# Performance work log

Hardware: AMD Instinct MI355X
Metric: run time of the kernel (lower is better)

Reference implementation:

```python
import jax, jax.numpy as jnp
import numpy as np

N_NODES = 100000
N_EDGES = 1200000
N_GRAPHS = 2048
VOCAB = 10000
D = 64
C = 2


def setup_inputs() -> dict:
    key = jax.random.key(0)
    ks = jax.random.split(key, 12)
    x = jax.random.randint(ks[0], (N_NODES,), 0, VOCAB)
    edge_index = jax.random.randint(ks[1], (2, N_EDGES), 0, N_NODES)
    batch = jnp.sort(jax.random.randint(ks[2], (N_NODES,), 0, N_GRAPHS))
    s = 0.1
    return {
        'x': x,
        'edge_index': edge_index,
        'batch': batch,
        'emb': jax.random.normal(ks[3], (VOCAB, D), jnp.float32) * s,
        'W1l': jax.random.normal(ks[4], (D, D), jnp.float32) * s,
        'b1l': jnp.zeros((D,), jnp.float32),
        'W1r': jax.random.normal(ks[5], (D, D), jnp.float32) * s,
        'W2l': jax.random.normal(ks[6], (D, D), jnp.float32) * s,
        'b2l': jnp.zeros((D,), jnp.float32),
        'W2r': jax.random.normal(ks[7], (D, D), jnp.float32) * s,
        'Wout': jax.random.normal(ks[8], (C, D), jnp.float32) * s,
        'bout': jnp.zeros((C,), jnp.float32),
    }


def _sage(h, src, dst, Wl, bl, Wr, n_nodes):
    # mean aggregation of source messages onto target nodes (PyG SAGEConv, aggr='mean')
    agg = jax.ops.segment_sum(h[src], dst, num_segments=n_nodes)  # [N, D]
    cnt = jax.ops.segment_sum(jnp.ones((src.shape[0],), h.dtype), dst, num_segments=n_nodes)
    agg = agg / jnp.maximum(cnt, 1.0)[:, None]
    # lin_l(agg) + lin_r(root); lin_l carries the bias, lin_r has none
    return agg @ Wl.T + bl + h @ Wr.T


def reference(x, edge_index, batch, emb, W1l, b1l, W1r, W2l, b2l, W2r, Wout, bout):
    src, dst = edge_index[0], edge_index[1]
    h = emb[x]                                   # [N, D] embedding lookup
    h = jax.nn.relu(_sage(h, src, dst, W1l, b1l, W1r, N_NODES))
    h = jax.nn.relu(_sage(h, src, dst, W2l, b2l, W2r, N_NODES))
    # global mean pool per graph
    pooled = jax.ops.segment_sum(h, batch, num_segments=N_GRAPHS)
    gcnt = jax.ops.segment_sum(jnp.ones((N_NODES,), h.dtype), batch, num_segments=N_GRAPHS)
    pooled = pooled / jnp.maximum(gcnt, 1.0)[:, None]
    return pooled @ Wout.T + bout                # [G, C]
```

## Files before the change

### kernel.cpp

```cpp
#include <hip/hip_runtime.h>

#define NN 100000
#define NE 1200000
#define NG 2048
#define VOCAB 10000
#define D 64
#define C 2

#define NBK 196
#define BSH 9
#define SLOT 7168

typedef _Float16 half8 __attribute__((ext_vector_type(8)));
typedef _Float16 half2 __attribute__((ext_vector_type(2)));

#if __has_builtin(__builtin_amdgcn_fdot2)
#define FDOT2(a, b, c) __builtin_amdgcn_fdot2((a), (b), (c), false)
#else
#define FDOT2(a, b, c) ((float)(a)[0] * (float)(b)[0] + (float)(a)[1] * (float)(b)[1] + (c))
#endif

__device__ __forceinline__ int atomAddI(int* p, int v) {
    return __hip_atomic_fetch_add(p, v, __ATOMIC_RELAXED, __HIP_MEMORY_SCOPE_AGENT);
}
__device__ __forceinline__ void atomAddF(float* p, float v) {
    __hip_atomic_fetch_add(p, v, __ATOMIC_RELAXED, __HIP_MEMORY_SCOPE_AGENT);
}

__global__ void __launch_bounds__(256) k_prep(const float4* __restrict__ emb4,
        half8* __restrict__ embh,
        const float* __restrict__ W1l, const float* __restrict__ W1r,
        const float* __restrict__ W2l, const float* __restrict__ W2r,
        half2* __restrict__ wp,
        const int* __restrict__ batch, int* __restrict__ gs) {
    int blk = blockIdx.x;
    if (blk < 313) {
        int i = blk * 256 + threadIdx.x;
        if (i >= VOCAB * 8) return;
        float4 a = emb4[(size_t)i * 2], b = emb4[(size_t)i * 2 + 1];
        half8 h;
        h[0] = (_Float16)a.x; h[1] = (_Float16)a.y; h[2] = (_Float16)a.z; h[3] = (_Float16)a.w;
        h[4] = (_Float16)b.x; h[5] = (_Float16)b.y; h[6] = (_Float16)b.z; h[7] = (_Float16)b.w;
        embh[i] = h;
    } else if (blk < 345) {
        int i = (blk - 313) * 256 + threadIdx.x;
        if (i >= 4 * 2048) return;
        int mat = i >> 11, idx = i & 2047;
        const float* W = (mat == 0) ? W1l : (mat == 1) ? W1r : (mat == 2) ? W2l : W2r;
        int row = idx >> 5, kk = idx & 31;
        half2 o;
        o[0] = (_Float16)W[row * 64 + 2 * kk];
        o[1] = (_Float16)W[row * 64 + 2 * kk + 1];
        wp[i] = o;
    } else {
        int n = (blk - 345) * 256 + threadIdx.x;
        if (n >= NN) return;
        int b = batch[n];
        if (n == 0) {
            for (int g = 0; g <= b; ++g) gs[g] = 0;
        } else {
            int bp = batch[n - 1];
            for (int g = bp + 1; g <= b; ++g) gs[g] = n;
        }
        if (n == NN - 1) {
            for (int g = b + 1; g <= NG; ++g) gs[g] = NN;
        }
    }
}

__global__ void __launch_bounds__(256) k_bucket(const int* __restrict__ src,
        const int* __restrict__ dst, int* __restrict__ bcur, unsigned* __restrict__ barr) {
    __shared__ int hcnt[NBK], hbase[NBK], hrank[NBK];
    int tid = threadIdx.x;
    if (tid < NBK) { hcnt[tid] = 0; hrank[tid] = 0; }
    __syncthreads();
    int per = (NE + gridDim.x - 1) / gridDim.x;
    int e0 = blockIdx.x * per, e1 = min(e0 + per, NE);
    for (int e = e0 + tid; e < e1; e += 256)
        atomicAdd(&hcnt[dst[e] >> BSH], 1);
    __syncthreads();
    if (tid < NBK) {
        int c = hcnt[tid];
        hbase[tid] = c ? atomAddI(&bcur[tid], c) : 0;
    }
    __syncthreads();
    for (int e = e0 + tid; e < e1; e += 256) {
        int d = dst[e], s = src[e];
        int b = d >> BSH;
        int r = atomicAdd(&hrank[b], 1);
        barr[(size_t)b * SLOT + hbase[b] + r] = ((unsigned)s << BSH) | (unsigned)(d & 511);
    }
}

__global__ void __launch_bounds__(256) k_bscan(const int* __restrict__ bcur,
        int* __restrict__ bstart, int* __restrict__ start) {
    __shared__ int sm[256];
    int t = threadIdx.x;
    int v0 = (t < NBK) ? bcur[t] : 0;
    sm[t] = v0;
    __syncthreads();
    for (int off = 1; off < 256; off <<= 1) {
        int v = (t >= off) ? sm[t - off] : 0;
        __syncthreads();
        sm[t] += v;
        __syncthreads();
    }
    if (t < NBK) bstart[t] = sm[t] - v0;
    if (t == 0) { bstart[NBK] = NE; start[NN] = NE; }
}

__global__ void __launch_bounds__(512) k_sortb(const int* __restrict__ bcur,
        const int* __restrict__ bstart, const unsigned* __restrict__ barr,
        const int* __restrict__ x,
        int* __restrict__ start, int* __restrict__ csr, unsigned short* __restrict__ xcsr) {
    __shared__ int cnt[512], loc[512], sm[512];
    int t = threadIdx.x;
    int b = blockIdx.x;
    cnt[t] = 0;
    __syncthreads();
    int count = bcur[b];
    int base  = bstart[b];
    const unsigned* bp = barr + (size_t)b * SLOT;
    for (int i = t; i < count; i += 512)
        atomicAdd(&cnt[bp[i] & 511], 1);
    __syncthreads();
    int own = cnt[t];
    sm[t] = own;
    __syncthreads();
    for (int off = 1; off < 512; off <<= 1) {
        int v = (t >= off) ? sm[t - off] : 0;
        __syncthreads();
        sm[t] += v;
        __syncthreads();
    }
    int ex = sm[t] - own;
    loc[t] = ex;
    int g0 = b << BSH;
    if (g0 + t < NN) start[g0 + t] = base + ex;
    __syncthreads();
    for (int i = t; i < count; i += 512) {
        unsigned p = bp[i];
        int r = atomicAdd(&loc[p & 511], 1);
        int sn = (int)(p >> BSH);
        csr[base + r]  = sn;
        xcsr[base + r] = (unsigned short)x[sn];
    }
}

template<typename IDX>
__device__ __forceinline__ half8 gather_sum(const IDX* __restrict__ idx,
        const half8* __restrict__ g, int f, int s0, int s1) {
    half8 acc = {};
    int i = s0;
    for (; i + 8 <= s1; i += 8) {
        half8 v0 = g[(size_t)idx[i]     * 8 + f];
        half8 v1 = g[(size_t)idx[i + 1] * 8 + f];
        half8 v2 = g[(size_t)idx[i + 2] * 8 + f];
        half8 v3 = g[(size_t)idx[i + 3] * 8 + f];
        half8 v4 = g[(size_t)idx[i + 4] * 8 + f];
        half8 v5 = g[(size_t)idx[i + 5] * 8 + f];
        half8 v6 = g[(size_t)idx[i + 6] * 8 + f];
        half8 v7 = g[(size_t)idx[i + 7] * 8 + f];
        acc += ((v0 + v1) + (v2 + v3)) + ((v4 + v5) + (v6 + v7));
    }
    if (i + 4 <= s1) {
        half8 v0 = g[(size_t)idx[i]     * 8 + f];
        half8 v1 = g[(size_t)idx[i + 1] * 8 + f];
        half8 v2 = g[(size_t)idx[i + 2] * 8 + f];
        half8 v3 = g[(size_t)idx[i + 3] * 8 + f];
        acc += (v0 + v1) + (v2 + v3);
        i += 4;
    }
    for (; i < s1; ++i) acc += g[(size_t)idx[i] * 8 + f];
    return acc;
}

__global__ void __launch_bounds__(256) k_l1(const int* __restrict__ start,
        const unsigned short* __restrict__ idx, const half8* __restrict__ embh,
        const int* __restrict__ x,
        const half2* __restrict__ wl, const float* __restrict__ bl,
        const half2* __restrict__ wr, half8* __restrict__ h1) {
    __shared__ half8 smA[64][8];
    int tid = threadIdx.x;
    int lane = tid & 63, wave = tid >> 6;

    float pf = 0.f;
    {
        int i = blockIdx.x * 256 + tid;
        if (i < VOCAB * 8) { float4 v = ((const float4*)embh)[i]; pf = v.x * 0.f; }
    }
    asm volatile("" : "+v"(pf));

    int f = lane & 7;
#pragma unroll
    for (int r = 0; r < 2; ++r) {
        int nl = r * 32 + wave * 8 + (lane >> 3);
        int n = blockIdx.x * 64 + nl;
        if (n < NN) {
            int s0 = start[n], s1 = start[n + 1];
            float inv = 1.0f / (float)max(s1 - s0, 1) + pf;
            half8 acc = gather_sum(idx, embh, f, s0, s1);
            half8 o;
#pragma unroll
            for (int k = 0; k < 8; ++k) o[k] = (_Float16)((float)acc[k] * inv);
            smA[nl][f ^ (nl & 7)] = o;
        }
    }
    __syncthreads();

    int h = __builtin_amdgcn_readfirstlane(wave);
    int nn = blockIdx.x * 64 + lane;
    bool valid = nn < NN;
    int n = valid ? nn : NN - 1;

    float acc[16];
#pragma unroll
    for (int d = 0; d < 16; ++d) acc[d] = bl[h * 16 + d];
    const half8* rp = embh + (size_t)x[n] * 8;
    const half2* wlH = wl + (size_t)h * 16 * 32;
    const half2* wrH = wr + (size_t)h * 16 * 32;

    half8 ah = smA[lane][0 ^ (lane & 7)];
    half8 rh = rp[0];
    for (int c = 0; c < 8; ++c) {
        half2 a2[4] = { __builtin_shufflevector(ah, ah, 0, 1),
                        __builtin_shufflevector(ah, ah, 2, 3),
                        __builtin_shufflevector(ah, ah, 4, 5),
                        __builtin_shufflevector(ah, ah, 6, 7) };
        half2 r2[4] = { __builtin_shufflevector(rh, rh, 0, 1),
                        __builtin_shufflevector(rh, rh, 2, 3),
                        __builtin_shufflevector(rh, rh, 4, 5),
                        __builtin_shufflevector(rh, rh, 6, 7) };
        if (c < 7) {
            ah = smA[lane][(c + 1) ^ (lane & 7)];
            rh = rp[c + 1];
        }
        const half2* wlc = wlH + c * 4;
        const half2* wrc = wrH + c * 4;
#pragma unroll
        for (int d = 0; d < 16; ++d) {
#pragma unroll
            for (int kk = 0; kk < 4; ++kk) {
                acc[d] = FDOT2(a2[kk], wlc[d * 32 + kk], acc[d]);
                acc[d] = FDOT2(r2[kk], wrc[d * 32 + kk], acc[d]);
            }
        }
    }

    if (valid) {
        half8 o0, o1;
#pragma unroll
        for (int k = 0; k < 8; ++k) {
            o0[k] = (_Float16)fmaxf(acc[k], 0.f);
            o1[k] = (_Float16)fmaxf(acc[8 + k], 0.f);
        }
        h1[(size_t)n * 8 + 2 * h]     = o0;
        h1[(size_t)n * 8 + 2 * h + 1] = o1;
    }
}

__global__ void __launch_bounds__(256) k_l2(const int* __restrict__ start,
        const int* __restrict__ idx, const half8* __restrict__ h1,
        const int* __restrict__ batch,
        const half2* __restrict__ wl, const float* __restrict__ bl,
        const half2* __restrict__ wr, float* __restrict__ pooled) {
    __shared__ half8 smA[64][8];
    int tid = threadIdx.x;
    int lane = tid & 63, wave = tid >> 6;

    int f = lane & 7;
#pragma unroll
    for (int r = 0; r < 2; ++r) {
        int nl = r * 32 + wave * 8 + (lane >> 3);
        int n = blockIdx.x * 64 + nl;
        if (n < NN) {
            int s0 = start[n], s1 = start[n + 1];
            float inv = 1.0f / (float)max(s1 - s0, 1);
            half8 acc = gather_sum(idx, h1, f, s0, s1);
            half8 o;
#pragma unroll
            for (int k = 0; k < 8; ++k) o[k] = (_Float16)((float)acc[k] * inv);
            smA[nl][f ^ (nl & 7)] = o;
        }
    }
    __syncthreads();

    int h = __builtin_amdgcn_readfirstlane(wave);
    int nn = blockIdx.x * 64 + lane;
    bool valid = nn < NN;
    int n = valid ? nn : NN - 1;

    float acc[16];
#pragma unroll
    for (int d = 0; d < 16; ++d) acc[d] = bl[h * 16 + d];
    const half8* rp = h1 + (size_t)n * 8;
    const half2* wlH = wl + (size_t)h * 16 * 32;
    const half2* wrH = wr + (size_t)h * 16 * 32;

    half8 ah = smA[lane][0 ^ (lane & 7)];
    half8 rh = rp[0];
    for (int c = 0; c < 8; ++c) {
        half2 a2[4] = { __builtin_shufflevector(ah, ah, 0, 1),
                        __builtin_shufflevector(ah, ah, 2, 3),
                        __builtin_shufflevector(ah, ah, 4, 5),
                        __builtin_shufflevector(ah, ah, 6, 7) };
        half2 r2[4] = { __builtin_shufflevector(rh, rh, 0, 1),
                        __builtin_shufflevector(rh, rh, 2, 3),
                        __builtin_shufflevector(rh, rh, 4, 5),
                        __builtin_shufflevector(rh, rh, 6, 7) };
        if (c < 7) {
            ah = smA[lane][(c + 1) ^ (lane & 7)];
            rh = rp[c + 1];
        }
        const half2* wlc = wlH + c * 4;
        const half2* wrc = wrH + c * 4;
#pragma unroll
        for (int d = 0; d < 16; ++d) {
#pragma unroll
            for (int kk = 0; kk < 4; ++kk) {
                acc[d] = FDOT2(a2[kk], wlc[d * 32 + kk], acc[d]);
                acc[d] = FDOT2(r2[kk], wrc[d * 32 + kk], acc[d]);
            }
        }
    }

    int g = batch[n];
    int g1  = __shfl_up(g, 1);
    int g2  = __shfl_up(g, 2);
    int g4  = __shfl_up(g, 4);
    int g8  = __shfl_up(g, 8);
    int g16 = __shfl_up(g, 16);
    int g32 = __shfl_up(g, 32);
    bool s1  = (lane >= 1)  && (g1 == g);
    bool s2  = (lane >= 2)  && (g2 == g);
    bool s4  = (lane >= 4)  && (g4 == g);
    bool s8  = (lane >= 8)  && (g8 == g);
    bool s16 = (lane >= 16) && (g16 == g);
    bool s32 = (lane >= 32) && (g32 == g);
    int gn = __shfl_down(g, 1);
    bool isLast = (lane == 63) || (gn != g);
    float* pg = pooled + (size_t)g * D + h * 16;
#pragma unroll
    for (int d = 0; d < 16; ++d) {
        float v = valid ? fmaxf(acc[d], 0.f) : 0.f;
        float t;
        t = __shfl_up(v, 1);  v += s1  ? t : 0.f;
        t = __shfl_up(v, 2);  v += s2  ? t : 0.f;
        t = __shfl_up(v, 4);  v += s4  ? t : 0.f;
        t = __shfl_up(v, 8);  v += s8  ? t : 0.f;
        t = __shfl_up(v, 16); v += s16 ? t : 0.f;
        t = __shfl_up(v, 32); v += s32 ? t : 0.f;
        if (isLast) atomAddF(pg + d, v);
    }
}

__global__ void __launch_bounds__(256) k_out(const int* __restrict__ gs,
        const float* __restrict__ pooled, const float* __restrict__ Wout,
        const float* __restrict__ bout, float* __restrict__ out) {
    int lane = threadIdx.x & 63;
    int wave = threadIdx.x >> 6;
    int g = blockIdx.x * 4 + wave;
    int s0 = gs[g], s1 = gs[g + 1];
    float p = pooled[(size_t)g * D + lane] / (float)max(s1 - s0, 1);
    float c0 = p * Wout[lane];
    float c1 = p * Wout[D + lane];
#pragma unroll
    for (int off = 32; off > 0; off >>= 1) {
        c0 += __shfl_down(c0, off, 64);
        c1 += __shfl_down(c1, off, 64);
    }
    if (lane == 0) {
        out[g * C + 0] = c0 + bout[0];
        out[g * C + 1] = c1 + bout[1];
    }
}

extern "C" void kernel_launch(void* const* d_in, const int* in_sizes, int n_in,
                              void* d_out, int out_size, void* d_ws, size_t ws_size,
                              hipStream_t stream) {
    const int*   x     = (const int*)d_in[0];
    const int*   src   = (const int*)d_in[1];
    const int*   dst   = src + NE;
    const int*   batch = (const int*)d_in[2];
    const float* emb   = (const float*)d_in[3];
    const float* W1l   = (const float*)d_in[4];
    const float* b1l   = (const float*)d_in[5];
    const float* W1r   = (const float*)d_in[6];
    const float* W2l   = (const float*)d_in[7];
    const float* b2l   = (const float*)d_in[8];
    const float* W2r   = (const float*)d_in[9];
    const float* Wout  = (const float*)d_in[10];
    const float* bout  = (const float*)d_in[11];
    float* out = (float*)d_out;

    _Float16* T0h  = (_Float16*)d_ws;
    _Float16* embh = T0h + (size_t)NN * 64;
    _Float16* wpck = embh + (size_t)VOCAB * 64;
    float* pooled  = (float*)(wpck + 16384);
    int* bcur   = (int*)(pooled + (size_t)NG * 64);
    int* bstart = bcur + NBK;
    int* startA = bstart + NBK + 1;
    int* gs     = startA + NN + 1;
    int* csr    = gs + NG + 1;
    unsigned short* xcsr = (unsigned short*)(csr + NE);
    unsigned* barr = (unsigned*)(xcsr + NE);
    half2* wp = (half2*)wpck;

    hipMemsetAsync(pooled, 0, ((size_t)NG * 64 + NBK) * sizeof(float), stream);

    k_prep  <<<736, 256, 0, stream>>>((const float4*)emb, (half8*)embh,
                                      W1l, W1r, W2l, W2r, wp, batch, gs);
    k_bucket<<<384, 256, 0, stream>>>(src, dst, bcur, barr);
    k_bscan <<<1, 256, 0, stream>>>(bcur, bstart, startA);
    k_sortb <<<NBK, 512, 0, stream>>>(bcur, bstart, barr, x, startA, csr, xcsr);

    int fusedGrid = (NN + 63) / 64;
    k_l1<<<fusedGrid, 256, 0, stream>>>(startA, xcsr, (const half8*)embh, x,
                                        wp, b1l, wp + 2048, (half8*)T0h);
    k_l2<<<fusedGrid, 256, 0, stream>>>(startA, csr, (const half8*)T0h, batch,
                                        wp + 4096, b2l, wp + 6144, pooled);

    k_out<<<NG / 4, 256, 0, stream>>>(gs, pooled, Wout, bout, out);
}
```

Measured before the change: 205.5 us.

## Gather layer-2 neighbours from an FP8 copy and fold bucketing into the prep kernel

Layer 1 now writes an extra FP8 copy of its output, and layer 2 gathers neighbour features from that 8-bit copy with fp32 accumulation. This halves the bytes of the dominant random gather. Separately, the edge bucketing kernel is merged into the prep kernel as extra blocks, and the bucket-offset scan moves into each sort block, which removes two launches. The FP8 quantisation adds precision loss in the layer-2 mean, and every sort block now repeats a small scan.

```diff
diff --git a/kernel.cpp b/kernel.cpp
--- a/kernel.cpp
+++ b/kernel.cpp
@@ -13,6 +13,8 @@
 
 typedef _Float16 half8 __attribute__((ext_vector_type(8)));
 typedef _Float16 half2 __attribute__((ext_vector_type(2)));
+typedef float floatx2 __attribute__((ext_vector_type(2)));
+typedef unsigned int u32;
 
 #if __has_builtin(__builtin_amdgcn_fdot2)
 #define FDOT2(a, b, c) __builtin_amdgcn_fdot2((a), (b), (c), false)
@@ -20,6 +22,41 @@
 #define FDOT2(a, b, c) ((float)(a)[0] * (float)(b)[0] + (float)(a)[1] * (float)(b)[1] + (c))
 #endif
 
+#if __has_builtin(__builtin_amdgcn_cvt_pk_fp8_f32) && __has_builtin(__builtin_amdgcn_cvt_pk_f32_fp8)
+#define HAVE_HW_FP8 1
+#endif
+
+__device__ __forceinline__ u32 pk_fp8(float a, float b, float c, float d) {
+#ifdef HAVE_HW_FP8
+    int v = 0;
+    v = __builtin_amdgcn_cvt_pk_fp8_f32(a, b, v, false);
+    v = __builtin_amdgcn_cvt_pk_fp8_f32(c, d, v, true);
+    return (u32)v;
+#else
+    float v4[4] = {a, b, c, d};
+    u32 r = 0;
+#pragma unroll
+    for (int j = 0; j < 4; ++j) {
+        unsigned short hb = __builtin_bit_cast(unsigned short, (_Float16)v4[j]);
+        r |= (u32)((unsigned short)(hb + 0x80) >> 8) << (8 * j);
+    }
+    return r;
+#endif
+}
+__device__ __forceinline__ void unpk_fp8(u32 v, float* o) {
+#ifdef HAVE_HW_FP8
+    floatx2 lo = __builtin_amdgcn_cvt_pk_f32_fp8(v, false);
+    floatx2 hi = __builtin_amdgcn_cvt_pk_f32_fp8(v, true);
+    o[0] = lo[0]; o[1] = lo[1]; o[2] = hi[0]; o[3] = hi[1];
+#else
+#pragma unroll
+    for (int j = 0; j < 4; ++j) {
+        unsigned short hb = (unsigned short)(((v >> (8 * j)) & 0xff) << 8);
+        o[j] = (float)__builtin_bit_cast(_Float16, hb);
+    }
+#endif
+}
+
 __device__ __forceinline__ int atomAddI(int* p, int v) {
     return __hip_atomic_fetch_add(p, v, __ATOMIC_RELAXED, __HIP_MEMORY_SCOPE_AGENT);
 }
@@ -27,15 +64,18 @@
     __hip_atomic_fetch_add(p, v, __ATOMIC_RELAXED, __HIP_MEMORY_SCOPE_AGENT);
 }
 
-__global__ void __launch_bounds__(256) k_prep(const float4* __restrict__ emb4,
+__global__ void __launch_bounds__(256) k_prepb(const float4* __restrict__ emb4,
         half8* __restrict__ embh,
         const float* __restrict__ W1l, const float* __restrict__ W1r,
         const float* __restrict__ W2l, const float* __restrict__ W2r,
         half2* __restrict__ wp,
-        const int* __restrict__ batch, int* __restrict__ gs) {
+        const int* __restrict__ batch, int* __restrict__ gs,
+        const int* __restrict__ src, const int* __restrict__ dst,
+        int* __restrict__ bcur, unsigned* __restrict__ barr) {
     int blk = blockIdx.x;
+    int tid = threadIdx.x;
     if (blk < 313) {
-        int i = blk * 256 + threadIdx.x;
+        int i = blk * 256 + tid;
         if (i >= VOCAB * 8) return;
         float4 a = emb4[(size_t)i * 2], b = emb4[(size_t)i * 2 + 1];
         half8 h;
@@ -43,7 +83,7 @@
         h[4] = (_Float16)b.x; h[5] = (_Float16)b.y; h[6] = (_Float16)b.z; h[7] = (_Float16)b.w;
         embh[i] = h;
     } else if (blk < 345) {
-        int i = (blk - 313) * 256 + threadIdx.x;
+        int i = (blk - 313) * 256 + tid;
         if (i >= 4 * 2048) return;
         int mat = i >> 11, idx = i & 2047;
         const float* W = (mat == 0) ? W1l : (mat == 1) ? W1r : (mat == 2) ? W2l : W2r;
@@ -52,8 +92,8 @@
         o[0] = (_Float16)W[row * 64 + 2 * kk];
         o[1] = (_Float16)W[row * 64 + 2 * kk + 1];
         wp[i] = o;
-    } else {
-        int n = (blk - 345) * 256 + threadIdx.x;
+    } else if (blk < 736) {
+        int n = (blk - 345) * 256 + tid;
         if (n >= NN) return;
         int b = batch[n];
         if (n == 0) {
@@ -65,61 +105,47 @@
         if (n == NN - 1) {
             for (int g = b + 1; g <= NG; ++g) gs[g] = NN;
         }
-    }
-}
-
-__global__ void __launch_bounds__(256) k_bucket(const int* __restrict__ src,
-        const int* __restrict__ dst, int* __restrict__ bcur, unsigned* __restrict__ barr) {
-    __shared__ int hcnt[NBK], hbase[NBK], hrank[NBK];
-    int tid = threadIdx.x;
-    if (tid < NBK) { hcnt[tid] = 0; hrank[tid] = 0; }
-    __syncthreads();
-    int per = (NE + gridDim.x - 1) / gridDim.x;
-    int e0 = blockIdx.x * per, e1 = min(e0 + per, NE);
-    for (int e = e0 + tid; e < e1; e += 256)
-        atomicAdd(&hcnt[dst[e] >> BSH], 1);
-    __syncthreads();
-    if (tid < NBK) {
-        int c = hcnt[tid];
-        hbase[tid] = c ? atomAddI(&bcur[tid], c) : 0;
-    }
-    __syncthreads();
-    for (int e = e0 + tid; e < e1; e += 256) {
-        int d = dst[e], s = src[e];
-        int b = d >> BSH;
-        int r = atomicAdd(&hrank[b], 1);
-        barr[(size_t)b * SLOT + hbase[b] + r] = ((unsigned)s << BSH) | (unsigned)(d & 511);
-    }
-}
-
-__global__ void __launch_bounds__(256) k_bscan(const int* __restrict__ bcur,
-        int* __restrict__ bstart, int* __restrict__ start) {
-    __shared__ int sm[256];
-    int t = threadIdx.x;
-    int v0 = (t < NBK) ? bcur[t] : 0;
-    sm[t] = v0;
-    __syncthreads();
-    for (int off = 1; off < 256; off <<= 1) {
-        int v = (t >= off) ? sm[t - off] : 0;
-        __syncthreads();
-        sm[t] += v;
-        __syncthreads();
-    }
-    if (t < NBK) bstart[t] = sm[t] - v0;
-    if (t == 0) { bstart[NBK] = NE; start[NN] = NE; }
+    } else {
+        __shared__ int hcnt[NBK], hbase[NBK], hrank[NBK];
+        if (tid < NBK) { hcnt[tid] = 0; hrank[tid] = 0; }
+        __syncthreads();
+        int bb = blk - 736;
+        int per = NE / 384;
+        int e0 = bb * per, e1 = e0 + per;
+        for (int e = e0 + tid; e < e1; e += 256)
+            atomicAdd(&hcnt[dst[e] >> BSH], 1);
+        __syncthreads();
+        if (tid < NBK) {
+            int c = hcnt[tid];
+            hbase[tid] = c ? atomAddI(&bcur[tid], c) : 0;
+        }
+        __syncthreads();
+        for (int e = e0 + tid; e < e1; e += 256) {
+            int d = dst[e], s = src[e];
+            int b = d >> BSH;
+            int r = atomicAdd(&hrank[b], 1);
+            barr[(size_t)b * SLOT + hbase[b] + r] = ((unsigned)s << BSH) | (unsigned)(d & 511);
+        }
+    }
 }
 
 __global__ void __launch_bounds__(512) k_sortb(const int* __restrict__ bcur,
-        const int* __restrict__ bstart, const unsigned* __restrict__ barr,
-        const int* __restrict__ x,
+        const unsigned* __restrict__ barr, const int* __restrict__ x,
         int* __restrict__ start, int* __restrict__ csr, unsigned short* __restrict__ xcsr) {
     __shared__ int cnt[512], loc[512], sm[512];
     int t = threadIdx.x;
     int b = blockIdx.x;
+    sm[t] = (t < b && t < NBK) ? bcur[t] : 0;
     cnt[t] = 0;
     __syncthreads();
+    for (int off = 1; off < 512; off <<= 1) {
+        int v = (t >= off) ? sm[t - off] : 0;
+        __syncthreads();
+        sm[t] += v;
+        __syncthreads();
+    }
+    int base = sm[511];
     int count = bcur[b];
-    int base  = bstart[b];
     const unsigned* bp = barr + (size_t)b * SLOT;
     for (int i = t; i < count; i += 512)
         atomicAdd(&cnt[bp[i] & 511], 1);
@@ -137,6 +163,7 @@
     loc[t] = ex;
     int g0 = b << BSH;
     if (g0 + t < NN) start[g0 + t] = base + ex;
+    if (b == NBK - 1 && t == 0) start[NN] = NE;
     __syncthreads();
     for (int i = t; i < count; i += 512) {
         unsigned p = bp[i];
@@ -175,11 +202,18 @@
     return acc;
 }
 
+__device__ __forceinline__ void acc_fp8(uint2 v, float* a) {
+    float t0[4], t1[4];
+    unpk_fp8(v.x, t0); unpk_fp8(v.y, t1);
+    a[0] += t0[0]; a[1] += t0[1]; a[2] += t0[2]; a[3] += t0[3];
+    a[4] += t1[0]; a[5] += t1[1]; a[6] += t1[2]; a[7] += t1[3];
+}
+
 __global__ void __launch_bounds__(256) k_l1(const int* __restrict__ start,
         const unsigned short* __restrict__ idx, const half8* __restrict__ embh,
         const int* __restrict__ x,
         const half2* __restrict__ wl, const float* __restrict__ bl,
-        const half2* __restrict__ wr, half8* __restrict__ h1) {
+        const half2* __restrict__ wr, half8* __restrict__ h1, u32* __restrict__ h8) {
     __shared__ half8 smA[64][8];
     int tid = threadIdx.x;
     int lane = tid & 63, wave = tid >> 6;
@@ -248,20 +282,28 @@
     }
 
     if (valid) {
+        float rl[16];
+#pragma unroll
+        for (int d = 0; d < 16; ++d) rl[d] = fmaxf(acc[d], 0.f);
         half8 o0, o1;
 #pragma unroll
         for (int k = 0; k < 8; ++k) {
-            o0[k] = (_Float16)fmaxf(acc[k], 0.f);
-            o1[k] = (_Float16)fmaxf(acc[8 + k], 0.f);
+            o0[k] = (_Float16)rl[k];
+            o1[k] = (_Float16)rl[8 + k];
         }
         h1[(size_t)n * 8 + 2 * h]     = o0;
         h1[(size_t)n * 8 + 2 * h + 1] = o1;
+        u32* h8r = h8 + (size_t)n * 16 + h * 4;
+        h8r[0] = pk_fp8(rl[0],  rl[1],  rl[2],  rl[3]);
+        h8r[1] = pk_fp8(rl[4],  rl[5],  rl[6],  rl[7]);
+        h8r[2] = pk_fp8(rl[8],  rl[9],  rl[10], rl[11]);
+        h8r[3] = pk_fp8(rl[12], rl[13], rl[14], rl[15]);
     }
 }
 
 __global__ void __launch_bounds__(256) k_l2(const int* __restrict__ start,
         const int* __restrict__ idx, const half8* __restrict__ h1,
-        const int* __restrict__ batch,
+        const uint2* __restrict__ h8, const int* __restrict__ batch,
         const half2* __restrict__ wl, const float* __restrict__ bl,
         const half2* __restrict__ wr, float* __restrict__ pooled) {
     __shared__ half8 smA[64][8];
@@ -276,10 +318,32 @@
         if (n < NN) {
             int s0 = start[n], s1 = start[n + 1];
             float inv = 1.0f / (float)max(s1 - s0, 1);
-            half8 acc = gather_sum(idx, h1, f, s0, s1);
+            float a[8] = {0.f, 0.f, 0.f, 0.f, 0.f, 0.f, 0.f, 0.f};
+            int i = s0;
+            for (; i + 8 <= s1; i += 8) {
+                uint2 v0 = h8[(size_t)idx[i]     * 8 + f];
+                uint2 v1 = h8[(size_t)idx[i + 1] * 8 + f];
+                uint2 v2 = h8[(size_t)idx[i + 2] * 8 + f];
+                uint2 v3 = h8[(size_t)idx[i + 3] * 8 + f];
+                uint2 v4 = h8[(size_t)idx[i + 4] * 8 + f];
+                uint2 v5 = h8[(size_t)idx[i + 5] * 8 + f];
+                uint2 v6 = h8[(size_t)idx[i + 6] * 8 + f];
+                uint2 v7 = h8[(size_t)idx[i + 7] * 8 + f];
+                acc_fp8(v0, a); acc_fp8(v1, a); acc_fp8(v2, a); acc_fp8(v3, a);
+                acc_fp8(v4, a); acc_fp8(v5, a); acc_fp8(v6, a); acc_fp8(v7, a);
+            }
+            if (i + 4 <= s1) {
+                uint2 v0 = h8[(size_t)idx[i]     * 8 + f];
+                uint2 v1 = h8[(size_t)idx[i + 1] * 8 + f];
+                uint2 v2 = h8[(size_t)idx[i + 2] * 8 + f];
+                uint2 v3 = h8[(size_t)idx[i + 3] * 8 + f];
+                acc_fp8(v0, a); acc_fp8(v1, a); acc_fp8(v2, a); acc_fp8(v3, a);
+                i += 4;
+            }
+            for (; i < s1; ++i) acc_fp8(h8[(size_t)idx[i] * 8 + f], a);
             half8 o;
 #pragma unroll
-            for (int k = 0; k < 8; ++k) o[k] = (_Float16)((float)acc[k] * inv);
+            for (int k = 0; k < 8; ++k) o[k] = (_Float16)(a[k] * inv);
             smA[nl][f ^ (nl & 7)] = o;
         }
     }
@@ -394,12 +458,12 @@
     float* out = (float*)d_out;
 
     _Float16* T0h  = (_Float16*)d_ws;
-    _Float16* embh = T0h + (size_t)NN * 64;
+    u32*      h8   = (u32*)(T0h + (size_t)NN * 64);
+    _Float16* embh = (_Float16*)(h8 + (size_t)NN * 16);
     _Float16* wpck = embh + (size_t)VOCAB * 64;
     float* pooled  = (float*)(wpck + 16384);
     int* bcur   = (int*)(pooled + (size_t)NG * 64);
-    int* bstart = bcur + NBK;
-    int* startA = bstart + NBK + 1;
+    int* startA = bcur + NBK;
     int* gs     = startA + NN + 1;
     int* csr    = gs + NG + 1;
     unsigned short* xcsr = (unsigned short*)(csr + NE);
@@ -408,16 +472,16 @@
 
     hipMemsetAsync(pooled, 0, ((size_t)NG * 64 + NBK) * sizeof(float), stream);
 
-    k_prep  <<<736, 256, 0, stream>>>((const float4*)emb, (half8*)embh,
-                                      W1l, W1r, W2l, W2r, wp, batch, gs);
-    k_bucket<<<384, 256, 0, stream>>>(src, dst, bcur, barr);
-    k_bscan <<<1, 256, 0, stream>>>(bcur, bstart, startA);
-    k_sortb <<<NBK, 512, 0, stream>>>(bcur, bstart, barr, x, startA, csr, xcsr);
+    k_prepb<<<1120, 256, 0, stream>>>((const float4*)emb, (half8*)embh,
+                                      W1l, W1r, W2l, W2r, wp, batch, gs,
+                                      src, dst, bcur, barr);
+    k_sortb<<<NBK, 512, 0, stream>>>(bcur, barr, x, startA, csr, xcsr);
 
     int fusedGrid = (NN + 63) / 64;
     k_l1<<<fusedGrid, 256, 0, stream>>>(startA, xcsr, (const half8*)embh, x,
-                                        wp, b1l, wp + 2048, (half8*)T0h);
-    k_l2<<<fusedGrid, 256, 0, stream>>>(startA, csr, (const half8*)T0h, batch,
+                                        wp, b1l, wp + 2048, (half8*)T0h, h8);
+    k_l2<<<fusedGrid, 256, 0, stream>>>(startA, csr, (const half8*)T0h,
+                                        (const uint2*)h8, batch,
                                         wp + 4096, b2l, wp + 6144, pooled);
 
     k_out<<<NG / 4, 256, 0, stream>>>(gs, pooled, Wout, bout, out);
```

Result: no change. 204.3 us (-0.6%).
